# Performance work log

Measured on AMD Instinct MI355X. Metric: run time of the kernel, lower is better.

## Reference

```python
import jax, jax.numpy as jnp
import numpy as np

GCE_Q = 0.7  # GeneralizedCELoss q
EPS = 1e-8
N, D, C = 2048, 1024, 10


def setup_inputs() -> dict:
    key = jax.random.key(0)
    ks = jax.random.split(key, 7)
    return {
        "z_c": jax.random.normal(ks[0], (N, D), dtype=jnp.float32),
        "z_b": jax.random.normal(ks[1], (N, D), dtype=jnp.float32),
        "Wc": jax.random.normal(ks[2], (C, D), dtype=jnp.float32) * 0.03,
        "bc": jax.random.normal(ks[3], (C,), dtype=jnp.float32) * 0.01,
        "Wb": jax.random.normal(ks[4], (C, D), dtype=jnp.float32) * 0.03,
        "bb": jax.random.normal(ks[5], (C,), dtype=jnp.float32) * 0.01,
        "y": jax.random.randint(ks[6], (N,), 0, C, dtype=jnp.int32),
    }


def reference(z_c, z_b, Wc, bc, Wb, bb, y):
    """Fused FuseCausal.combination + get_weight('ratio') + amplified loss.

    Pair (i, j) uses z = z_c[i] + z_b[j]; CE targets y[i], GCE targets y[j].
    Since Linear is affine: logits[i,j] = (z_c @ W.T)[i] + (z_b @ W.T)[j] + b,
    which avoids materializing the [N, N, D] pair tensor (same math).
    Returns loss_amp [N, N] = w * CE_pc + (1 - w) * GCE_pb,
    with w = stop_grad(CE_pb / (CE_pc + CE_pb + eps)).
    """
    n = y.shape[0]
    yi = jnp.broadcast_to(y[:, None, None], (n, n, 1))  # target y[i] per pair
    yj = jnp.broadcast_to(y[None, :, None], (n, n, 1))  # target y[j] per pair

    # causal head: all-pairs log-softmax, CE with target y[i]
    logits_c = (z_c @ Wc.T)[:, None, :] + (z_b @ Wc.T)[None, :, :] + bc  # [N,N,C]
    logsm_c = jax.nn.log_softmax(logits_c, axis=-1)
    ce_pc = -jnp.take_along_axis(logsm_c, yi, axis=-1)[..., 0]  # [N,N]

    # bias head: CE with target y[i], GCE with target y[j]
    logits_b = (z_c @ Wb.T)[:, None, :] + (z_b @ Wb.T)[None, :, :] + bb
    logsm_b = jax.nn.log_softmax(logits_b, axis=-1)
    ce_pb = -jnp.take_along_axis(logsm_b, yi, axis=-1)[..., 0]
    logp_yj = jnp.take_along_axis(logsm_b, yj, axis=-1)[..., 0]
    # GCE: CE(logits_b, y[j]) * detach(p_yj ** q)
    gce_pb = (-logp_yj) * jax.lax.stop_gradient(jnp.exp(logp_yj) ** GCE_Q)

    # get_weight('ratio') on detached losses
    w = jax.lax.stop_gradient(ce_pb / (ce_pc + ce_pb + EPS))
    loss_amp = w * ce_pc + (1.0 - w) * gce_pb  # [N,N]
    return loss_amp
```

## Files before the change

### kernel.cpp

```cpp
#include <hip/hip_runtime.h>

#define NN 2048
#define DD 1024
#define CC 10
#define RS 16
#define ICH 16
#define GCE_Q_ 0.7f
#define EPS_ 1e-8f

#define OFF_EAc 0
#define OFF_EAb 32768
#define OFF_Abr 65536
#define OFF_EBc 98304
#define OFF_EBb 131072
#define OFF_BcT 163840
#define OFF_BbT 184320
#define OFF_IA  204800
#define OFF_JS  212992

__global__ __launch_bounds__(256) void prep_kernel(
    const float* __restrict__ z_c, const float* __restrict__ z_b,
    const float* __restrict__ Wc, const float* __restrict__ bc,
    const float* __restrict__ Wb, const float* __restrict__ bb,
    const int* __restrict__ y, float* __restrict__ ws)
{
  const int t = threadIdx.x;
  const int d0 = t * 4;

  float4 wcr[CC], wbr[CC];
#pragma unroll
  for (int k = 0; k < CC; ++k) {
    wcr[k] = *(const float4*)(Wc + k * DD + d0);
    wbr[k] = *(const float4*)(Wb + k * DD + d0);
  }

  const int rowBase = blockIdx.x * 8;
  const bool isB = rowBase >= NN;
  const float* __restrict__ z = isB ? z_b : z_c;
  const int r0 = isB ? (rowBase - NN) : rowBase;

  __shared__ float red[8][64][20];
  __shared__ float sums[8][20];

  float4 zv = *(const float4*)(z + (size_t)r0 * DD + d0);
  for (int rr = 0; rr < 8; ++rr) {
    float4 zn = zv;
    if (rr < 7) zn = *(const float4*)(z + (size_t)(r0 + rr + 1) * DD + d0);

    float pc[CC], pb[CC];
#pragma unroll
    for (int k = 0; k < CC; ++k) {
      pc[k] = fmaf(zv.x, wcr[k].x, fmaf(zv.y, wcr[k].y, fmaf(zv.z, wcr[k].z, zv.w * wcr[k].w)));
      pb[k] = fmaf(zv.x, wbr[k].x, fmaf(zv.y, wbr[k].y, fmaf(zv.z, wbr[k].z, zv.w * wbr[k].w)));
    }
#pragma unroll
    for (int m = 1; m <= 2; m <<= 1) {
#pragma unroll
      for (int k = 0; k < CC; ++k) {
        pc[k] += __shfl_xor(pc[k], m, 64);
        pb[k] += __shfl_xor(pb[k], m, 64);
      }
    }
    if ((t & 3) == 0) {
      float* dst = &red[rr][t >> 2][0];
#pragma unroll
      for (int k = 0; k < CC; ++k) { dst[k] = pc[k]; dst[CC + k] = pb[k]; }
    }
    zv = zn;
  }
  __syncthreads();

  if (t < 160) {
    const int rr = t / 20;
    const int kk = t % 20;
    float s0 = 0.f, s1 = 0.f, s2 = 0.f, s3 = 0.f;
#pragma unroll
    for (int p = 0; p < 64; p += 4) {
      s0 += red[rr][p + 0][kk];
      s1 += red[rr][p + 1][kk];
      s2 += red[rr][p + 2][kk];
      s3 += red[rr][p + 3][kk];
    }
    float s = (s0 + s1) + (s2 + s3);
    if (!isB) s += (kk < CC) ? bc[kk] : bb[kk - CC];
    sums[rr][kk] = s;
  }
  __syncthreads();

  if (t < 160) {
    const int rr = t / 20;
    const int kk = t % 20;
    const int head = kk / CC;
    const int k = kk % CC;
    const int row = r0 + rr;
    float m = -1e30f;
#pragma unroll
    for (int q = 0; q < CC; ++q) m = fmaxf(m, sums[rr][head * CC + q]);
    const float v = sums[rr][kk];
    const float e = __expf(v - m);
    if (!isB) {
      if (head == 0) {
        ws[OFF_EAc + row * RS + k] = e;
      } else {
        ws[OFF_EAb + row * RS + k] = e;
        ws[OFF_Abr + row * RS + k] = v;
      }
    } else {
      if (head == 0) {
        ws[OFF_EBc + row * RS + k] = e;
        ws[OFF_BcT + k * NN + row] = v;
      } else {
        ws[OFF_EBb + row * RS + k] = e;
        ws[OFF_BbT + k * NN + row] = v;
      }
    }
    if (kk == 0) {
      const int yr = y[row];
      float m0 = -1e30f, m1 = -1e30f;
#pragma unroll
      for (int q = 0; q < CC; ++q) {
        m0 = fmaxf(m0, sums[rr][q]);
        m1 = fmaxf(m1, sums[rr][CC + q]);
      }
      float4 v4;
      if (!isB) {
        v4 = make_float4(m0, m1, sums[rr][yr], sums[rr][CC + yr]);
        *(float4*)(ws + OFF_IA + row * 4) = v4;
      } else {
        v4 = make_float4(m0, m1, sums[rr][CC + yr], 0.f);
        *(float4*)(ws + OFF_JS + row * 4) = v4;
      }
    }
  }
}

__global__ __launch_bounds__(256) void pair_kernel(
    const float* __restrict__ ws, const int* __restrict__ y,
    float* __restrict__ out)
{
  const float* __restrict__ EAc = ws + OFF_EAc;
  const float* __restrict__ EAb = ws + OFF_EAb;
  const float* __restrict__ Abr = ws + OFF_Abr;
  const float* __restrict__ EBc = ws + OFF_EBc;
  const float* __restrict__ EBb = ws + OFF_EBb;
  const float* __restrict__ BcT = ws + OFF_BcT;
  const float* __restrict__ BbT = ws + OFF_BbT;
  const float* __restrict__ IA  = ws + OFF_IA;
  const float* __restrict__ JS  = ws + OFF_JS;

  const int j = blockIdx.x * 256 + threadIdx.x;

  float ebc[CC], ebb[CC];
#pragma unroll
  for (int k = 0; k < CC; ++k) {
    ebc[k] = EBc[j * RS + k];
    ebb[k] = EBb[j * RS + k];
  }
  const float4 js = *(const float4*)(JS + j * 4);
  const float mBc = js.x, mBb = js.y, Bby = js.z;
  const int yj = y[j];

  const int iBase = __builtin_amdgcn_readfirstlane(blockIdx.y * ICH);
  for (int ii = 0; ii < ICH; ++ii) {
    const int i = iBase + ii;
    float eac[CC], eab[CC];
#pragma unroll
    for (int k = 0; k < CC; ++k) {
      eac[k] = EAc[i * RS + k];
      eab[k] = EAb[i * RS + k];
    }
    const float4 ia = *(const float4*)(IA + i * 4);
    const int yi = y[i];

    float sc = 0.f, sb = 0.f;
#pragma unroll
    for (int k = 0; k < CC; ++k) {
      sc = fmaf(eac[k], ebc[k], sc);
      sb = fmaf(eab[k], ebb[k], sb);
    }
    const float lse_c = ia.x + mBc + __logf(sc);
    const float lse_b = ia.y + mBb + __logf(sb);

    const float Bc_jyi = BcT[yi * NN + j];
    const float Bb_jyi = BbT[yi * NN + j];
    const float Ab_iyj = Abr[i * RS + yj];

    const float ce_pc = lse_c - ia.z - Bc_jyi;
    const float ce_pb = lse_b - ia.w - Bb_jyi;
    const float logp_yj = Ab_iyj + Bby - lse_b;
    const float gce = -logp_yj * __expf(GCE_Q_ * logp_yj);
    const float w = ce_pb * __builtin_amdgcn_rcpf(ce_pc + ce_pb + EPS_);
    out[(size_t)i * NN + j] = fmaf(w, ce_pc - gce, gce);
  }
}

extern "C" void kernel_launch(void* const* d_in, const int* in_sizes, int n_in,
                              void* d_out, int out_size, void* d_ws, size_t ws_size,
                              hipStream_t stream) {
  const float* z_c = (const float*)d_in[0];
  const float* z_b = (const float*)d_in[1];
  const float* Wc  = (const float*)d_in[2];
  const float* bc  = (const float*)d_in[3];
  const float* Wb  = (const float*)d_in[4];
  const float* bb  = (const float*)d_in[5];
  const int*   y   = (const int*)d_in[6];
  float* out = (float*)d_out;
  float* ws  = (float*)d_ws;

  prep_kernel<<<dim3(512), dim3(256), 0, stream>>>(z_c, z_b, Wc, bc, Wb, bb, y, ws);
  pair_kernel<<<dim3(8, NN / ICH), dim3(256), 0, stream>>>(ws, y, out);
}
```

Before: 103.7 us.

## Pack per-row i records, compute two j per thread, use DPP reductions

Packs the per-i softmax data (exps, raw logits, max-minus-target terms, label) into one 48-float record per row, which removes the separate y[i] and IA loads. Each pair-kernel thread now handles two adjacent j columns with float2 stores and float2 gathers of the transposed B logits, so per-i loads are shared across two outputs. The i-chunk per block is halved to keep the grid size. Prep-kernel cross-lane sums switch from shfl_xor to DPP quad permutes. The cost is more registers per thread and a changed grid shape.

```diff
diff --git a/kernel.cpp b/kernel.cpp
--- a/kernel.cpp
+++ b/kernel.cpp
@@ -4,19 +4,29 @@
 #define DD 1024
 #define CC 10
 #define RS 16
-#define ICH 16
+#define RREC 48
+#define ICH 8
+#define J2 2
 #define GCE_Q_ 0.7f
 #define EPS_ 1e-8f
 
-#define OFF_EAc 0
-#define OFF_EAb 32768
-#define OFF_Abr 65536
+#define OFF_IREC 0
 #define OFF_EBc 98304
 #define OFF_EBb 131072
-#define OFF_BcT 163840
-#define OFF_BbT 184320
-#define OFF_IA  204800
-#define OFF_JS  212992
+#define OFF_JS  163840
+#define OFF_BcT 172032
+#define OFF_BbT 192512
+
+__device__ __forceinline__ float dpp_xor1_add(float x) {
+  int xi = __float_as_int(x);
+  int s = __builtin_amdgcn_update_dpp(xi, xi, 0xB1, 0xF, 0xF, false);
+  return x + __int_as_float(s);
+}
+__device__ __forceinline__ float dpp_xor2_add(float x) {
+  int xi = __float_as_int(x);
+  int s = __builtin_amdgcn_update_dpp(xi, xi, 0x4E, 0xF, 0xF, false);
+  return x + __int_as_float(s);
+}
 
 __global__ __launch_bounds__(256) void prep_kernel(
     const float* __restrict__ z_c, const float* __restrict__ z_b,
@@ -54,13 +64,10 @@
       pb[k] = fmaf(zv.x, wbr[k].x, fmaf(zv.y, wbr[k].y, fmaf(zv.z, wbr[k].z, zv.w * wbr[k].w)));
     }
 #pragma unroll
-    for (int m = 1; m <= 2; m <<= 1) {
-#pragma unroll
-      for (int k = 0; k < CC; ++k) {
-        pc[k] += __shfl_xor(pc[k], m, 64);
-        pb[k] += __shfl_xor(pb[k], m, 64);
-      }
-    }
+    for (int k = 0; k < CC; ++k) { pc[k] = dpp_xor1_add(pc[k]); pb[k] = dpp_xor1_add(pb[k]); }
+#pragma unroll
+    for (int k = 0; k < CC; ++k) { pc[k] = dpp_xor2_add(pc[k]); pb[k] = dpp_xor2_add(pb[k]); }
+
     if ((t & 3) == 0) {
       float* dst = &red[rr][t >> 2][0];
 #pragma unroll
@@ -98,12 +105,13 @@
     for (int q = 0; q < CC; ++q) m = fmaxf(m, sums[rr][head * CC + q]);
     const float v = sums[rr][kk];
     const float e = __expf(v - m);
+    float* rec = ws + OFF_IREC + row * RREC;
     if (!isB) {
       if (head == 0) {
-        ws[OFF_EAc + row * RS + k] = e;
+        rec[k] = e;
       } else {
-        ws[OFF_EAb + row * RS + k] = e;
-        ws[OFF_Abr + row * RS + k] = v;
+        rec[10 + k] = e;
+        rec[20 + k] = v;
       }
     } else {
       if (head == 0) {
@@ -122,13 +130,13 @@
         m0 = fmaxf(m0, sums[rr][q]);
         m1 = fmaxf(m1, sums[rr][CC + q]);
       }
-      float4 v4;
       if (!isB) {
-        v4 = make_float4(m0, m1, sums[rr][yr], sums[rr][CC + yr]);
-        *(float4*)(ws + OFF_IA + row * 4) = v4;
+        *(float4*)(rec + 32) = make_float4(m0 - sums[rr][yr],
+                                           m1 - sums[rr][CC + yr],
+                                           m1, __int_as_float(yr));
       } else {
-        v4 = make_float4(m0, m1, sums[rr][CC + yr], 0.f);
-        *(float4*)(ws + OFF_JS + row * 4) = v4;
+        *(float4*)(ws + OFF_JS + row * 4) = make_float4(m0, m1,
+                                                        sums[rr][CC + yr] - m1, 0.f);
       }
     }
   }
@@ -138,59 +146,63 @@
     const float* __restrict__ ws, const int* __restrict__ y,
     float* __restrict__ out)
 {
-  const float* __restrict__ EAc = ws + OFF_EAc;
-  const float* __restrict__ EAb = ws + OFF_EAb;
-  const float* __restrict__ Abr = ws + OFF_Abr;
   const float* __restrict__ EBc = ws + OFF_EBc;
   const float* __restrict__ EBb = ws + OFF_EBb;
+  const float* __restrict__ JS  = ws + OFF_JS;
   const float* __restrict__ BcT = ws + OFF_BcT;
   const float* __restrict__ BbT = ws + OFF_BbT;
-  const float* __restrict__ IA  = ws + OFF_IA;
-  const float* __restrict__ JS  = ws + OFF_JS;
-
-  const int j = blockIdx.x * 256 + threadIdx.x;
-
-  float ebc[CC], ebb[CC];
-#pragma unroll
-  for (int k = 0; k < CC; ++k) {
-    ebc[k] = EBc[j * RS + k];
-    ebb[k] = EBb[j * RS + k];
-  }
-  const float4 js = *(const float4*)(JS + j * 4);
-  const float mBc = js.x, mBb = js.y, Bby = js.z;
-  const int yj = y[j];
+
+  const int j0 = (blockIdx.x * 256 + threadIdx.x) * J2;
+
+  float ebc[J2][CC], ebb[J2][CC];
+  float4 js[J2];
+  int yj[J2];
+#pragma unroll
+  for (int jj = 0; jj < J2; ++jj) {
+#pragma unroll
+    for (int k = 0; k < CC; ++k) {
+      ebc[jj][k] = EBc[(j0 + jj) * RS + k];
+      ebb[jj][k] = EBb[(j0 + jj) * RS + k];
+    }
+    js[jj] = *(const float4*)(JS + (j0 + jj) * 4);
+    yj[jj] = y[j0 + jj];
+  }
 
   const int iBase = __builtin_amdgcn_readfirstlane(blockIdx.y * ICH);
+#pragma unroll 2
   for (int ii = 0; ii < ICH; ++ii) {
     const int i = iBase + ii;
+    const float* __restrict__ rec = ws + OFF_IREC + i * RREC;
     float eac[CC], eab[CC];
 #pragma unroll
-    for (int k = 0; k < CC; ++k) {
-      eac[k] = EAc[i * RS + k];
-      eab[k] = EAb[i * RS + k];
-    }
-    const float4 ia = *(const float4*)(IA + i * 4);
-    const int yi = y[i];
-
-    float sc = 0.f, sb = 0.f;
-#pragma unroll
-    for (int k = 0; k < CC; ++k) {
-      sc = fmaf(eac[k], ebc[k], sc);
-      sb = fmaf(eab[k], ebb[k], sb);
-    }
-    const float lse_c = ia.x + mBc + __logf(sc);
-    const float lse_b = ia.y + mBb + __logf(sb);
-
-    const float Bc_jyi = BcT[yi * NN + j];
-    const float Bb_jyi = BbT[yi * NN + j];
-    const float Ab_iyj = Abr[i * RS + yj];
-
-    const float ce_pc = lse_c - ia.z - Bc_jyi;
-    const float ce_pb = lse_b - ia.w - Bb_jyi;
-    const float logp_yj = Ab_iyj + Bby - lse_b;
-    const float gce = -logp_yj * __expf(GCE_Q_ * logp_yj);
-    const float w = ce_pb * __builtin_amdgcn_rcpf(ce_pc + ce_pb + EPS_);
-    out[(size_t)i * NN + j] = fmaf(w, ce_pc - gce, gce);
+    for (int k = 0; k < CC; ++k) { eac[k] = rec[k]; eab[k] = rec[10 + k]; }
+    const float4 ia = *(const float4*)(rec + 32);
+    const int yi = __float_as_int(ia.w);
+
+    const float2 bcv = *(const float2*)(BcT + yi * NN + j0);
+    const float2 bbv = *(const float2*)(BbT + yi * NN + j0);
+
+    float outv[J2];
+#pragma unroll
+    for (int jj = 0; jj < J2; ++jj) {
+      float sc = 0.f, sb = 0.f;
+#pragma unroll
+      for (int k = 0; k < CC; ++k) {
+        sc = fmaf(eac[k], ebc[jj][k], sc);
+        sb = fmaf(eab[k], ebb[jj][k], sb);
+      }
+      const float lc = __logf(sc);
+      const float lb = __logf(sb);
+      const float bc_ = jj ? bcv.y : bcv.x;
+      const float bb_ = jj ? bbv.y : bbv.x;
+      const float ce_pc = ia.x + js[jj].x + lc - bc_;
+      const float ce_pb = ia.y + js[jj].y + lb - bb_;
+      const float logp  = rec[20 + yj[jj]] + js[jj].z - ia.z - lb;
+      const float gce   = -logp * __expf(GCE_Q_ * logp);
+      const float w     = ce_pb * __builtin_amdgcn_rcpf(ce_pc + ce_pb + EPS_);
+      outv[jj] = fmaf(w, ce_pc - gce, gce);
+    }
+    *(float2*)(out + (size_t)i * NN + j0) = make_float2(outv[0], outv[1]);
   }
 }
 
@@ -208,5 +220,5 @@
   float* ws  = (float*)d_ws;
 
   prep_kernel<<<dim3(512), dim3(256), 0, stream>>>(z_c, z_b, Wc, bc, Wb, bb, y, ws);
-  pair_kernel<<<dim3(8, NN / ICH), dim3(256), 0, stream>>>(ws, y, out);
-}
+  pair_kernel<<<dim3(NN / (256 * J2), NN / ICH), dim3(256), 0, stream>>>(ws, y, out);
+}
```

After: 102.4 us. Within noise of the previous version (-1.3%).
